# Kernel optimization log

Hardware: AMD Instinct MI355X
Metric: run time of the kernel (lower is better)

## Reference

```python
import jax, jax.numpy as jnp
import numpy as np

T, B, C, H, W, L, K = 8, 8, 64, 96, 96, 2, 3


def _conv(x, w):
    # x: [B,C,H,W], w: [O,I,K,K], SAME padding, stride 1
    return jax.lax.conv_general_dilated(
        x, w, window_strides=(1, 1), padding='SAME',
        dimension_numbers=('NCHW', 'OIHW', 'NCHW'))


def setup_inputs() -> dict:
    key = jax.random.key(0)
    ks = jax.random.split(key, 17)
    wscale = 0.04  # ~ 1/sqrt(64*9) fan-in
    out = {'x': jax.random.normal(ks[0], (T, B, C, H, W), jnp.float32)}
    wnames = ['wxi', 'whi', 'wci', 'wxf', 'whf', 'wcf', 'wxc', 'whc',
              'wxo', 'who', 'wco']
    for i, n in enumerate(wnames):
        out[n] = jax.random.normal(ks[1 + i], (L, C, C, K, K), jnp.float32) * wscale
    bnames = ['b_i', 'b_f', 'b_c', 'b_o']
    for i, n in enumerate(bnames):
        out[n] = jax.random.normal(ks[12 + i], (L, C), jnp.float32) * 0.01
    return out


def reference(x, wxi, whi, wci, wxf, whf, wcf, wxc, whc, wxo, who, wco,
              b_i, b_f, b_c, b_o):
    # x: [T,B,C,H,W]. Peephole Conv-LSTM; note original module's quirk:
    # output gate uses w_hc (with its bias) applied to the NEW cell state.
    hs = cs = None
    for l in range(L):
        Wxi, Whi, Wci = wxi[l], whi[l], wci[l]
        Wxf, Whf, Wcf = wxf[l], whf[l], wcf[l]
        Wxc, Whc = wxc[l], whc[l]
        Wxo, Who, Wco = wxo[l], who[l], wco[l]
        bi = b_i[l][None, :, None, None]
        bf = b_f[l][None, :, None, None]
        bc = b_c[l][None, :, None, None]
        bo = b_o[l][None, :, None, None]

        def step(carry, xt, Wxi=Wxi, Whi=Whi, Wci=Wci, Wxf=Wxf, Whf=Whf,
                 Wcf=Wcf, Wxc=Wxc, Whc=Whc, Wxo=Wxo, Who=Who,
                 bi=bi, bf=bf, bc=bc, bo=bo):
            h, c = carry
            i = jax.nn.sigmoid(_conv(xt, Wxi) + _conv(h, Whi) + bi + _conv(c, Wci))
            f = jax.nn.sigmoid(_conv(xt, Wxf) + _conv(h, Whf) + bf + _conv(c, Wcf))
            c_t = jnp.tanh(_conv(xt, Wxc) + _conv(h, Whc) + bc)
            c_new = c_t * i + c * f
            # faithful to source: w_hc (with its bias) on the new cell state
            o = jax.nn.sigmoid(_conv(xt, Wxo) + _conv(h, Who) + bo
                               + _conv(c_new, Whc) + bc)
            h_new = o * jnp.tanh(c_new)
            return (h_new, c_new), (h_new, c_new)

        h0 = jnp.zeros((x.shape[1], C, H, W), x.dtype)
        c0 = jnp.zeros((x.shape[1], C, H, W), x.dtype)
        _, (hs, cs) = jax.lax.scan(step, (h0, c0), x)
        x = hs  # next layer consumes this layer's hidden sequence
    return hs, cs  # each [T,B,C,H,W]
```

## Files before the change

kernel.cpp:

```cpp
#include <hip/hip_runtime.h>
#include <math.h>

#define TT 8
#define BB 8
#define CC 64
#define HH 96
#define WW 96
#define LL 2
#define HW   (HH * WW)
#define CHW  (CC * HW)
#define BCHW (BB * CHW)
#define TBCHW (TT * BCHW)
#define WSZ  (CC * CC * 9)

typedef _Float16 f16;
typedef __attribute__((ext_vector_type(8))) _Float16 f16x8;
typedef __attribute__((ext_vector_type(4))) _Float16 f16x4;
typedef __attribute__((ext_vector_type(4))) float f32x4;

__device__ __forceinline__ float sigmoidf_(float x) {
    return 1.0f / (1.0f + __expf(-x));
}


#define SLOT_B   9834496ull
#define PLANE_B  1229312ull
#define SLOT_F   (SLOT_B / 2)
#define GPLANE_F 4718592ull
#define WT_F     36864

struct WPtrs { const float* p[10]; };

__device__ __forceinline__ void gl_lds16(const void* g, void* lds_base) {
    __builtin_amdgcn_global_load_lds(
        (const __attribute__((address_space(1))) unsigned int*)g,
        (__attribute__((address_space(3))) unsigned int*)lds_base, 16, 0, 0);
}

__global__ __launch_bounds__(256) void wprep(WPtrs wsrcs, f16* Wf) {
    const int tap = blockIdx.x, ti = blockIdx.y, l = blockIdx.z;
    const float* src = wsrcs.p[ti] + l * WSZ;
    f16* dst = Wf + (size_t)(l * 10 + ti) * WT_F;
    for (int r = 0; r < 16; ++r) {
        int lin = r * 256 + threadIdx.x;
        int co = lin >> 6, ci = lin & 63;
        float v = src[(co * 64 + ci) * 9 + tap];
        int half = ci >> 5, e = ci & 31, s = e >> 3;
        int p = (s ^ co) & 3;
        dst[((half * 9 + tap) * 64 + co) * 32 + p * 8 + (e & 7)] = (f16)v;
    }
}

__global__ __launch_bounds__(256) void bzero(char* slots) {
    unsigned u = blockIdx.x * 256 + threadIdx.x;
    if (u >= 248320u) return;
    unsigned plane = u / 3104u;
    unsigned r = u % 3104u;
    unsigned i = r >> 3, c = r & 7;
    int y, x;
    if (i < 98)       { y = 0;           x = i; }
    else if (i < 196) { y = 97;          x = i - 98; }
    else if (i < 292) { y = i - 196 + 1; x = 0; }
    else              { y = i - 292 + 1; x = 97; }
    uint4 z = make_uint4(0, 0, 0, 0);
    *(uint4*)(slots + (size_t)plane * PLANE_B + (size_t)(y * 98 + x) * 128 + c * 16) = z;
}

__global__ __launch_bounds__(256) void xprep(const float* __restrict__ x, f16* slots) {
    const int t = blockIdx.y;
    const int b = blockIdx.x / 96, y = blockIdx.x % 96;
    f16* slot = slots + (size_t)t * SLOT_F;
    for (int r = 0; r < 3; ++r) {
        int u = r * 256 + threadIdx.x;
        int px = u >> 3, c = u & 7;
        int half = c >> 2, p = c & 3;
        int sc = (p ^ (px + 1)) & 3;
        int ci0 = half * 32 + sc * 8;
        const float* sp = x + ((((size_t)t * BB + b) * CC + ci0) * HH + y) * WW + px;
        union { f16 h[8]; uint4 q; } pk;
#pragma unroll
        for (int j = 0; j < 8; ++j) pk.h[j] = (f16)sp[(size_t)j * HW];
        f16* dp = slot + ((size_t)b * 9604 + (y + 1) * 98 + (px + 1)) * 64 + half * 32 + p * 8;
        *(uint4*)dp = pk.q;
    }
}

__device__ __forceinline__ void stage_phase(const char* __restrict__ xb_h, int y0,
                                            const char* __restrict__ wsec_h,
                                            int tid, f16* Xs, f16* Wl) {
    const int w = tid >> 6, lane = tid & 63;
    const char* xc = xb_h + (size_t)y0 * 12544;
    const int cb = w * 588;
#pragma unroll
    for (int i = 0; i < 9; ++i) {
        const int c = cb + i * 64 + lane;
        gl_lds16(xc + (size_t)(c >> 2) * 128 + (c & 3) * 16,
                 (char*)Xs + (size_t)(cb + i * 64) * 16);
    }
    if (lane < 12) {
        const int c = cb + 576 + lane;
        gl_lds16(xc + (size_t)(c >> 2) * 128 + (c & 3) * 16,
                 (char*)Xs + (size_t)(cb + 576) * 16);
    }
    const int cw = w * 576;
#pragma unroll
    for (int i = 0; i < 9; ++i) {
        gl_lds16(wsec_h + (size_t)(cw + i * 64 + lane) * 16,
                 (char*)Wl + (size_t)(cw + i * 64) * 16);
    }
}

__device__ __forceinline__ void mfma_phase(const f16* Xs, const f16* Wl,
                                           int w, int aBase, int d0, int d1, int d2,
                                           f32x4 acc[4][6]) {
#pragma unroll
    for (int tap = 0; tap < 9; ++tap) {
        const int dy = tap / 3, dx = tap % 3;
        const f16* Ar = &Wl[tap * 2048 + aBase];
        f16x8 a0 = *(const f16x8*)(Ar);
        f16x8 a1 = *(const f16x8*)(Ar + 512);
        f16x8 a2 = *(const f16x8*)(Ar + 1024);
        f16x8 a3 = *(const f16x8*)(Ar + 1536);
        const int doff = (dx == 0) ? d0 : (dx == 1) ? d1 : d2;
        const f16* Br = &Xs[(w + dy) * 3136 + doff];
#pragma unroll
        for (int nt = 0; nt < 6; ++nt) {
            f16x8 bf = *(const f16x8*)(Br + nt * 512);
            acc[0][nt] = __builtin_amdgcn_mfma_f32_16x16x32_f16(a0, bf, acc[0][nt], 0, 0, 0);
            acc[1][nt] = __builtin_amdgcn_mfma_f32_16x16x32_f16(a1, bf, acc[1][nt], 0, 0, 0);
            acc[2][nt] = __builtin_amdgcn_mfma_f32_16x16x32_f16(a2, bf, acc[2][nt], 0, 0, 0);
            acc[3][nt] = __builtin_amdgcn_mfma_f32_16x16x32_f16(a3, bf, acc[3][nt], 0, 0, 0);
        }
    }
}

struct GArgsN {
    const f16* in[3];
    const f16* w[4][3];
    f16* G;
};

__global__ __launch_bounds__(256) void gates_n(GArgsN A) {
    __shared__ __align__(16) f16 Xs[18816];
    __shared__ __align__(16) f16 Wl[18432];
    const int g = blockIdx.z, b = blockIdx.y, y0 = blockIdx.x * 4;
    const int tid = threadIdx.x, w = tid >> 6, lane = tid & 63;
    const int pxl = lane & 15, kg = lane >> 4;

    const int aBase = pxl * 32 + (((kg ^ pxl) & 3) << 3);
    const int d0 = (pxl + 0) * 32 + (((kg ^ (pxl + 0)) & 3) << 3);
    const int d1 = (pxl + 1) * 32 + (((kg ^ (pxl + 1)) & 3) << 3);
    const int d2 = (pxl + 2) * 32 + (((kg ^ (pxl + 2)) & 3) << 3);

    f32x4 acc[4][6];
#pragma unroll
    for (int mt = 0; mt < 4; ++mt)
#pragma unroll
        for (int nt = 0; nt < 6; ++nt) acc[mt][nt] = (f32x4){0.f, 0.f, 0.f, 0.f};

    for (int s = 0; s < 3; ++s) {
        const f16* xin = A.in[s];
        const f16* wsec = A.w[g][s];
        if (!xin || !wsec) continue;
        const char* xb = (const char*)(xin + (size_t)b * 614656);
        for (int h = 0; h < 2; ++h) {
            __syncthreads();
            stage_phase(xb + h * 64, y0, (const char*)(wsec + h * 18432), tid, Xs, Wl);
            __syncthreads();
            mfma_phase(Xs, Wl, w, aBase, d0, d1, d2, acc);
        }
    }

    f16* Gg = A.G + (size_t)g * GPLANE_F + ((size_t)b * 9216 + (y0 + w) * 96) * 64;
#pragma unroll
    for (int mt = 0; mt < 4; ++mt)
#pragma unroll
        for (int nt = 0; nt < 6; ++nt) {
            union { f16 h[4]; uint2 q; } pk;
#pragma unroll
            for (int r = 0; r < 4; ++r) pk.h[r] = (f16)acc[mt][nt][r];
            *(uint2*)(Gg + (size_t)(nt * 16 + pxl) * 64 + mt * 16 + kg * 4) = pk.q;
        }
}

__global__ __launch_bounds__(256) void pointwise_n(const f16* __restrict__ G,
                                                   const f16* __restrict__ cprev,
                                                   const float* __restrict__ bi,
                                                   const float* __restrict__ bf,
                                                   const float* __restrict__ bc,
                                                   f16* __restrict__ cnew,
                                                   float* __restrict__ cs_out) {
    const int b = blockIdx.y;
    const int u = blockIdx.x * 256 + threadIdx.x;
    const int pix = u >> 3, o = u & 7;
    const int ci0 = o * 8;
    const f16x8 gi = *(const f16x8*)(G + ((size_t)b * 9216 + pix) * 64 + ci0);
    const f16x8 gf = *(const f16x8*)(G + GPLANE_F + ((size_t)b * 9216 + pix) * 64 + ci0);
    const f16x8 gc = *(const f16x8*)(G + 2 * GPLANE_F + ((size_t)b * 9216 + pix) * 64 + ci0);
    const int py = pix / 96 + 1, pxp = pix % 96 + 1;
    const size_t pad_off = ((size_t)b * 9604 + py * 98 + pxp) * 64;
    const int half = o >> 2, p = ((o & 3) ^ pxp) & 3;
    const size_t sw_off = pad_off + half * 32 + p * 8;
    f16x8 cp = (f16x8)(_Float16)0.f;
    if (cprev) cp = *(const f16x8*)(cprev + sw_off);
    union { f16 h[8]; uint4 q; } outp;
    float cv[8];
#pragma unroll
    for (int j = 0; j < 8; ++j) {
        float vbi = bi[ci0 + j], vbf = bf[ci0 + j], vbc = bc[ci0 + j];
        float c = tanhf((float)gc[j] + vbc) * sigmoidf_((float)gi[j] + vbi)
                + (float)cp[j] * sigmoidf_((float)gf[j] + vbf);
        cv[j] = c;
        outp.h[j] = (f16)c;
    }
    *(uint4*)(cnew + sw_off) = outp.q;
    if (cs_out) {
        float* op = cs_out + (size_t)b * CHW + (size_t)ci0 * HW + pix;
#pragma unroll
        for (int j = 0; j < 8; ++j) op[(size_t)j * HW] = cv[j];
    }
}

__global__ __launch_bounds__(256) void out_n(const f16* __restrict__ cnew,
                                             const f16* __restrict__ whc,
                                             const f16* __restrict__ Go,
                                             const float* __restrict__ bo,
                                             const float* __restrict__ bc,
                                             f16* __restrict__ hslot,
                                             float* __restrict__ hs_out) {
    __shared__ __align__(16) f16 Xs[18816];
    __shared__ __align__(16) f16 Wl[18432];
    const int b = blockIdx.y, y0 = blockIdx.x * 4;
    const int tid = threadIdx.x, w = tid >> 6, lane = tid & 63;
    const int pxl = lane & 15, kg = lane >> 4;

    const int aBase = pxl * 32 + (((kg ^ pxl) & 3) << 3);
    const int d0 = (pxl + 0) * 32 + (((kg ^ (pxl + 0)) & 3) << 3);
    const int d1 = (pxl + 1) * 32 + (((kg ^ (pxl + 1)) & 3) << 3);
    const int d2 = (pxl + 2) * 32 + (((kg ^ (pxl + 2)) & 3) << 3);

    f32x4 acc[4][6];
#pragma unroll
    for (int mt = 0; mt < 4; ++mt)
#pragma unroll
        for (int nt = 0; nt < 6; ++nt) acc[mt][nt] = (f32x4){0.f, 0.f, 0.f, 0.f};

    const char* xb = (const char*)(cnew + (size_t)b * 614656);
    for (int h = 0; h < 2; ++h) {
        __syncthreads();
        stage_phase(xb + h * 64, y0, (const char*)(whc + h * 18432), tid, Xs, Wl);
        __syncthreads();
        mfma_phase(Xs, Wl, w, aBase, d0, d1, d2, acc);
    }

    const int y = y0 + w;
#pragma unroll
    for (int mt = 0; mt < 4; ++mt) {
        const int cob = mt * 16 + kg * 4;
        float vb[4];
#pragma unroll
        for (int r = 0; r < 4; ++r) vb[r] = bo[cob + r] + bc[cob + r];
        const int half = mt >> 1;
        const int sq = (mt * 2 + (kg >> 1)) & 3;
        const int lo4 = (kg & 1) * 4;
#pragma unroll
        for (int nt = 0; nt < 6; ++nt) {
            const int px = nt * 16 + pxl;
            const int pix = y * 96 + px;
            const size_t pad_off = ((size_t)b * 9604 + (y + 1) * 98 + (px + 1)) * 64;
            const int p = (sq ^ (px + 1)) & 3;
            const size_t qoff = pad_off + half * 32 + p * 8 + lo4;
            f16x4 cq = *(const f16x4*)(cnew + qoff);
            f16x4 gq = *(const f16x4*)(Go + ((size_t)b * 9216 + pix) * 64 + cob);
            union { f16 h[4]; uint2 q; } hq;
            float hv[4];
#pragma unroll
            for (int r = 0; r < 4; ++r) {
                float opre = acc[mt][nt][r] + (float)gq[r] + vb[r];
                hv[r] = sigmoidf_(opre) * tanhf((float)cq[r]);
                hq.h[r] = (f16)hv[r];
            }
            *(uint2*)(hslot + qoff) = hq.q;
            if (hs_out) {
                float* op = hs_out + (size_t)b * CHW + (size_t)cob * HW + pix;
#pragma unroll
                for (int r = 0; r < 4; ++r) op[(size_t)r * HW] = hv[r];
            }
        }
    }
}


#define XROW 3136
#define XSZ  (6 * XROW)
#define WROW 2048
#define WSZL (9 * WROW)

__device__ __forceinline__ void conv_section(
    const float* __restrict__ inb, const float* __restrict__ wp,
    int y0, int tid, f16* Xs, f16* Wl,
    int w, int aBase, int d0, int d1, int d2, f32x4 acc[4][6])
{
    for (int ci0 = 0; ci0 < 64; ci0 += 32) {
        __syncthreads();
        for (int i = tid; i < 9408; i += 256) {
            int x = i % 98; int r = i / 98; int yy = r % 6; int c2 = r / 6;
            int gy = y0 - 1 + yy, gx = x - 1;
            float v0 = 0.f, v1 = 0.f;
            if ((unsigned)gy < 96u && (unsigned)gx < 96u) {
                const float* p = inb + (size_t)(ci0 + 2 * c2) * HW + gy * WW + gx;
                v0 = p[0]; v1 = p[HW];
            }
            union { f16 h[2]; unsigned u; } pk;
            pk.h[0] = (f16)v0; pk.h[1] = (f16)v1;
            int e = 2 * c2;
            int idx = (yy * 98 + x) * 32 + ((((e >> 3) ^ x) & 3) << 3) + (e & 7);
            *(unsigned*)&Xs[idx] = pk.u;
        }
        for (int i = tid; i < 9216; i += 256) {
            int c2 = i & 15; int co = (i >> 4) & 63; int tap = i >> 10;
            const float* p = wp + ((size_t)co * CC + ci0 + 2 * c2) * 9 + tap;
            union { f16 h[2]; unsigned u; } pk;
            pk.h[0] = (f16)p[0]; pk.h[1] = (f16)p[9];
            int e = 2 * c2;
            int idx = tap * WROW + co * 32 + ((((e >> 3) ^ co) & 3) << 3) + (e & 7);
            *(unsigned*)&Wl[idx] = pk.u;
        }
        __syncthreads();
        mfma_phase(Xs, Wl, w, aBase, d0, d1, d2, acc);
    }
}

struct GArgs {
    const float* in[3];
    const float* w[4][3];
    f16* G;
};

__global__ __launch_bounds__(256) void gates_mfma(GArgs A) {
    __shared__ __align__(16) f16 Xs[XSZ];
    __shared__ __align__(16) f16 Wl[WSZL];
    const int g = blockIdx.z, b = blockIdx.y, y0 = blockIdx.x * 4;
    const int tid = threadIdx.x;
    const int w = tid >> 6, lane = tid & 63;
    const int pxl = lane & 15, kg = lane >> 4;
    const int aBase = pxl * 32 + (((kg ^ pxl) & 3) << 3);
    const int d0 = (pxl + 0) * 32 + (((kg ^ (pxl + 0)) & 3) << 3);
    const int d1 = (pxl + 1) * 32 + (((kg ^ (pxl + 1)) & 3) << 3);
    const int d2 = (pxl + 2) * 32 + (((kg ^ (pxl + 2)) & 3) << 3);
    f32x4 acc[4][6];
#pragma unroll
    for (int mt = 0; mt < 4; ++mt)
#pragma unroll
        for (int nt = 0; nt < 6; ++nt) acc[mt][nt] = (f32x4){0.f, 0.f, 0.f, 0.f};
    for (int s = 0; s < 3; ++s) {
        const float* inp = A.in[s];
        const float* wp = A.w[g][s];
        if (!inp || !wp) continue;
        conv_section(inp + (size_t)b * CHW, wp, y0, tid, Xs, Wl, w, aBase, d0, d1, d2, acc);
    }
    f16* Gp = A.G + (size_t)(g * BB + b) * CHW;
    const int y = y0 + w;
#pragma unroll
    for (int mt = 0; mt < 4; ++mt)
#pragma unroll
        for (int r = 0; r < 4; ++r) {
            const int co = mt * 16 + kg * 4 + r;
            f16* rp = Gp + (size_t)co * HW + y * WW + pxl;
#pragma unroll
            for (int nt = 0; nt < 6; ++nt) rp[nt * 16] = (f16)acc[mt][nt][r];
        }
}

__global__ __launch_bounds__(256) void pointwise_c(const f16* __restrict__ G,
                                                   const float* __restrict__ cprev,
                                                   const float* __restrict__ bi,
                                                   const float* __restrict__ bf,
                                                   const float* __restrict__ bc,
                                                   float* __restrict__ cnew) {
    int flat = (blockIdx.x * 256 + threadIdx.x) * 4;
    if (flat >= BCHW) return;
    int co = (flat / HW) & 63;
    f16x4 gi = *(const f16x4*)(G + flat);
    f16x4 gf = *(const f16x4*)(G + (size_t)BCHW + flat);
    f16x4 gc = *(const f16x4*)(G + 2 * (size_t)BCHW + flat);
    float4 cp = make_float4(0.f, 0.f, 0.f, 0.f);
    if (cprev) cp = *(const float4*)(cprev + flat);
    float vbi = bi[co], vbf = bf[co], vbc = bc[co];
    float4 r;
    r.x = tanhf((float)gc.x + vbc) * sigmoidf_((float)gi.x + vbi) + cp.x * sigmoidf_((float)gf.x + vbf);
    r.y = tanhf((float)gc.y + vbc) * sigmoidf_((float)gi.y + vbi) + cp.y * sigmoidf_((float)gf.y + vbf);
    r.z = tanhf((float)gc.z + vbc) * sigmoidf_((float)gi.z + vbi) + cp.z * sigmoidf_((float)gf.z + vbf);
    r.w = tanhf((float)gc.w + vbc) * sigmoidf_((float)gi.w + vbi) + cp.w * sigmoidf_((float)gf.w + vbf);
    *(float4*)(cnew + flat) = r;
}

__global__ __launch_bounds__(256) void out_mfma(const float* __restrict__ cnew,
                                                const float* __restrict__ wp,
                                                const f16* __restrict__ Go,
                                                const float* __restrict__ bo,
                                                const float* __restrict__ bc,
                                                float* __restrict__ hout) {
    __shared__ __align__(16) f16 Xs[XSZ];
    __shared__ __align__(16) f16 Wl[WSZL];
    const int b = blockIdx.y, y0 = blockIdx.x * 4;
    const int tid = threadIdx.x;
    const int w = tid >> 6, lane = tid & 63;
    const int pxl = lane & 15, kg = lane >> 4;
    const int aBase = pxl * 32 + (((kg ^ pxl) & 3) << 3);
    const int d0 = (pxl + 0) * 32 + (((kg ^ (pxl + 0)) & 3) << 3);
    const int d1 = (pxl + 1) * 32 + (((kg ^ (pxl + 1)) & 3) << 3);
    const int d2 = (pxl + 2) * 32 + (((kg ^ (pxl + 2)) & 3) << 3);
    f32x4 acc[4][6];
#pragma unroll
    for (int mt = 0; mt < 4; ++mt)
#pragma unroll
        for (int nt = 0; nt < 6; ++nt) acc[mt][nt] = (f32x4){0.f, 0.f, 0.f, 0.f};
    const float* cb = cnew + (size_t)b * CHW;
    conv_section(cb, wp, y0, tid, Xs, Wl, w, aBase, d0, d1, d2, acc);
    const f16* Gb = Go + (size_t)b * CHW;
    float* hb = hout + (size_t)b * CHW;
    const int y = y0 + w;
#pragma unroll
    for (int mt = 0; mt < 4; ++mt)
#pragma unroll
        for (int r = 0; r < 4; ++r) {
            const int co = mt * 16 + kg * 4 + r;
            const float vbv = bo[co] + bc[co];
            const size_t off0 = (size_t)co * HW + y * WW + pxl;
#pragma unroll
            for (int nt = 0; nt < 6; ++nt) {
                size_t off = off0 + nt * 16;
                float opre = acc[mt][nt][r] + (float)Gb[off] + vbv;
                hb[off] = sigmoidf_(opre) * tanhf(cb[off]);
            }
        }
}


extern "C" void kernel_launch(void* const* d_in, const int* in_sizes, int n_in,
                              void* d_out, int out_size, void* d_ws, size_t ws_size,
                              hipStream_t stream) {
    const float* x = (const float*)d_in[0];
    const float* w_[11];
    for (int i = 0; i < 11; ++i) w_[i] = (const float*)d_in[1 + i];
    const float* b_[4];
    for (int i = 0; i < 4; ++i) b_[i] = (const float*)d_in[12 + i];

    float* out = (float*)d_out;
    float* hs = out;
    float* cs = out + TBCHW;

    const size_t G_B = 4ull * GPLANE_F * 2ull;
    const size_t WF_B = 2ull * 10ull * WT_F * 2ull;
    const size_t NEED = 10ull * SLOT_B + G_B + WF_B;

    if (ws_size >= NEED) {
        char* ws = (char*)d_ws;
        f16* slots = (f16*)ws;
        f16* G = (f16*)(ws + 10ull * SLOT_B);
        f16* Wf = (f16*)(ws + 10ull * SLOT_B + G_B);

        WPtrs wps;
        for (int i = 0; i < 10; ++i) wps.p[i] = w_[i];

        wprep<<<dim3(9, 10, 2), 256, 0, stream>>>(wps, Wf);
        bzero<<<dim3(971), 256, 0, stream>>>((char*)slots);
        xprep<<<dim3(96 * BB, TT), 256, 0, stream>>>(x, slots);

        for (int l = 0; l < LL; ++l) {
            const f16* WT[10];
            for (int ti = 0; ti < 10; ++ti) WT[ti] = Wf + (size_t)(l * 10 + ti) * WT_F;
            const float* bi = b_[0] + l * CC;
            const float* bf = b_[1] + l * CC;
            const float* bc = b_[2] + l * CC;
            const float* bo = b_[3] + l * CC;

            for (int t = 0; t < TT; ++t) {
                f16* xt = slots + (size_t)t * SLOT_F;
                f16* hprev = (t == 0) ? nullptr : slots + (size_t)(t - 1) * SLOT_F;
                f16* cprev = (t == 0) ? nullptr
                                      : slots + (size_t)(8 + ((t - 1) & 1)) * SLOT_F;
                f16* cnew = slots + (size_t)(8 + (t & 1)) * SLOT_F;

                GArgsN a;
                a.in[0] = xt; a.in[1] = hprev; a.in[2] = cprev;
                a.w[0][0] = WT[0]; a.w[0][1] = WT[1]; a.w[0][2] = WT[2];
                a.w[1][0] = WT[3]; a.w[1][1] = WT[4]; a.w[1][2] = WT[5];
                a.w[2][0] = WT[6]; a.w[2][1] = WT[7]; a.w[2][2] = nullptr;
                a.w[3][0] = WT[8]; a.w[3][1] = WT[9]; a.w[3][2] = nullptr;
                a.G = G;
                gates_n<<<dim3(24, BB, 4), 256, 0, stream>>>(a);
                pointwise_n<<<dim3(288, BB), 256, 0, stream>>>(
                    G, cprev, bi, bf, bc, cnew,
                    (l == 1) ? (cs + (size_t)t * BCHW) : nullptr);
                out_n<<<dim3(24, BB), 256, 0, stream>>>(
                    cnew, WT[7], G + 3 * GPLANE_F, bo, bc,
                    xt,
                    (l == 1) ? (hs + (size_t)t * BCHW) : nullptr);
            }
        }
        return;
    }

    f16* G = (f16*)d_ws;
    float* c0 = (float*)d_ws + 2 * (size_t)BCHW;
    float* c1 = c0 + BCHW;

    for (int l = 0; l < LL; ++l) {
        const float* wxi = w_[0] + l * WSZ;
        const float* whi = w_[1] + l * WSZ;
        const float* wci = w_[2] + l * WSZ;
        const float* wxf = w_[3] + l * WSZ;
        const float* whf = w_[4] + l * WSZ;
        const float* wcf = w_[5] + l * WSZ;
        const float* wxc = w_[6] + l * WSZ;
        const float* whc = w_[7] + l * WSZ;
        const float* wxo = w_[8] + l * WSZ;
        const float* who = w_[9] + l * WSZ;
        const float* bi = b_[0] + l * CC;
        const float* bf = b_[1] + l * CC;
        const float* bc = b_[2] + l * CC;
        const float* bo = b_[3] + l * CC;

        for (int t = 0; t < TT; ++t) {
            const float* xt = (l == 0) ? (x + (size_t)t * BCHW) : (hs + (size_t)t * BCHW);
            const float* hprev = (t == 0) ? nullptr : (hs + (size_t)(t - 1) * BCHW);
            const float* cprev = (t == 0) ? nullptr
                : (l == 0 ? (((t - 1) & 1) ? c1 : c0) : (cs + (size_t)(t - 1) * BCHW));
            float* cnew = (l == 0) ? ((t & 1) ? c1 : c0) : (cs + (size_t)t * BCHW);

            GArgs a;
            a.in[0] = xt; a.in[1] = hprev; a.in[2] = cprev;
            a.w[0][0] = wxi; a.w[0][1] = whi; a.w[0][2] = wci;
            a.w[1][0] = wxf; a.w[1][1] = whf; a.w[1][2] = wcf;
            a.w[2][0] = wxc; a.w[2][1] = whc; a.w[2][2] = nullptr;
            a.w[3][0] = wxo; a.w[3][1] = who; a.w[3][2] = nullptr;
            a.G = G;
            gates_mfma<<<dim3(24, BB, 4), 256, 0, stream>>>(a);
            pointwise_c<<<dim3(BCHW / 1024), 256, 0, stream>>>(G, cprev, bi, bf, bc, cnew);
            out_mfma<<<dim3(24, BB), 256, 0, stream>>>(cnew, whc, G + (size_t)3 * BCHW,
                                                       bo, bc, hs + (size_t)t * BCHW);
        }
    }
}
```

Measured before the change: 1.815 ms.

## Prefetch conv weights through registers one phase ahead; use fast tanh

The per-phase LDS staging of weights is split out. Weights for the next phase are now loaded into registers while the current phase's MFMAs run, then written to LDS at the start of the next phase, overlapping weight fetch latency with compute. The t=0 null-pointer skipping is replaced by a zeroed slot that is re-zeroed at the start of each layer, so the kernels take fixed templated phase counts with no per-section branches. This does more convolution work at the first timestep. tanhf is replaced by an exp-based approximation in the pointwise and output kernels, which can lose accuracy or overflow to inf for large inputs, though the formula still saturates to ±1.

```diff
diff --git a/kernel.cpp b/kernel.cpp
--- a/kernel.cpp
+++ b/kernel.cpp
@@ -20,6 +20,10 @@
 
 __device__ __forceinline__ float sigmoidf_(float x) {
     return 1.0f / (1.0f + __expf(-x));
+}
+__device__ __forceinline__ float tanhf_(float x) {
+    float e = __expf(2.f * x);
+    return 1.f - 2.f / (e + 1.f);
 }
 
 
@@ -66,6 +70,11 @@
     *(uint4*)(slots + (size_t)plane * PLANE_B + (size_t)(y * 98 + x) * 128 + c * 16) = z;
 }
 
+__global__ __launch_bounds__(256) void zslot(char* slot) {
+    size_t off = ((size_t)blockIdx.x * 256 + threadIdx.x) * 16;
+    *(uint4*)(slot + off) = make_uint4(0, 0, 0, 0);
+}
+
 __global__ __launch_bounds__(256) void xprep(const float* __restrict__ x, f16* slots) {
     const int t = blockIdx.y;
     const int b = blockIdx.x / 96, y = blockIdx.x % 96;
@@ -85,10 +94,8 @@
     }
 }
 
-__device__ __forceinline__ void stage_phase(const char* __restrict__ xb_h, int y0,
-                                            const char* __restrict__ wsec_h,
-                                            int tid, f16* Xs, f16* Wl) {
-    const int w = tid >> 6, lane = tid & 63;
+__device__ __forceinline__ void stage_x(const char* __restrict__ xb_h, int y0,
+                                        int w, int lane, f16* Xs) {
     const char* xc = xb_h + (size_t)y0 * 12544;
     const int cb = w * 588;
 #pragma unroll
@@ -102,12 +109,20 @@
         gl_lds16(xc + (size_t)(c >> 2) * 128 + (c & 3) * 16,
                  (char*)Xs + (size_t)(cb + 576) * 16);
     }
-    const int cw = w * 576;
-#pragma unroll
-    for (int i = 0; i < 9; ++i) {
-        gl_lds16(wsec_h + (size_t)(cw + i * 64 + lane) * 16,
-                 (char*)Wl + (size_t)(cw + i * 64) * 16);
-    }
+}
+
+struct W9 { uint4 v[9]; };
+__device__ __forceinline__ W9 wload(const char* __restrict__ wsec_h, int cw, int lane) {
+    W9 r;
+#pragma unroll
+    for (int i = 0; i < 9; ++i)
+        r.v[i] = *(const uint4*)(wsec_h + (size_t)(cw + i * 64 + lane) * 16);
+    return r;
+}
+__device__ __forceinline__ void wstore(f16* Wl, const W9& r, int cw, int lane) {
+#pragma unroll
+    for (int i = 0; i < 9; ++i)
+        *(uint4*)((char*)Wl + (size_t)(cw + i * 64 + lane) * 16) = r.v[i];
 }
 
 __device__ __forceinline__ void mfma_phase(const f16* Xs, const f16* Wl,
@@ -134,6 +149,30 @@
     }
 }
 
+template<int NP>
+__device__ __forceinline__ void conv_pipe(const char* xb0, const char* xb1, const char* xb2,
+                                          const char* wp0, const char* wp1, const char* wp2,
+                                          int y0, int w, int lane, int cw,
+                                          f16* Xs, f16* Wl,
+                                          int aBase, int d0, int d1, int d2,
+                                          f32x4 acc[4][6]) {
+    W9 wreg = wload(wp0, cw, lane);
+#pragma unroll
+    for (int p = 0; p < NP; ++p) {
+        const char* xb_s = ((p >> 1) == 0) ? xb0 : ((p >> 1) == 1) ? xb1 : xb2;
+        __syncthreads();
+        wstore(Wl, wreg, cw, lane);
+        stage_x(xb_s + (p & 1) * 64, y0, w, lane, Xs);
+        __syncthreads();
+        if (p + 1 < NP) {
+            const int s1 = (p + 1) >> 1;
+            const char* wp_s = (s1 == 0) ? wp0 : (s1 == 1) ? wp1 : wp2;
+            wreg = wload(wp_s + ((p + 1) & 1) * 36864, cw, lane);
+        }
+        mfma_phase(Xs, Wl, w, aBase, d0, d1, d2, acc);
+    }
+}
+
 struct GArgsN {
     const f16* in[3];
     const f16* w[4][3];
@@ -146,6 +185,7 @@
     const int g = blockIdx.z, b = blockIdx.y, y0 = blockIdx.x * 4;
     const int tid = threadIdx.x, w = tid >> 6, lane = tid & 63;
     const int pxl = lane & 15, kg = lane >> 4;
+    const int cw = w * 576;
 
     const int aBase = pxl * 32 + (((kg ^ pxl) & 3) << 3);
     const int d0 = (pxl + 0) * 32 + (((kg ^ (pxl + 0)) & 3) << 3);
@@ -158,18 +198,19 @@
 #pragma unroll
         for (int nt = 0; nt < 6; ++nt) acc[mt][nt] = (f32x4){0.f, 0.f, 0.f, 0.f};
 
-    for (int s = 0; s < 3; ++s) {
-        const f16* xin = A.in[s];
-        const f16* wsec = A.w[g][s];
-        if (!xin || !wsec) continue;
-        const char* xb = (const char*)(xin + (size_t)b * 614656);
-        for (int h = 0; h < 2; ++h) {
-            __syncthreads();
-            stage_phase(xb + h * 64, y0, (const char*)(wsec + h * 18432), tid, Xs, Wl);
-            __syncthreads();
-            mfma_phase(Xs, Wl, w, aBase, d0, d1, d2, acc);
-        }
-    }
+    const char* xb0 = (const char*)(A.in[0] + (size_t)b * 614656);
+    const char* xb1 = (const char*)(A.in[1] + (size_t)b * 614656);
+    const char* xb2 = (const char*)(A.in[2] + (size_t)b * 614656);
+    const char* wp0 = (const char*)A.w[g][0];
+    const char* wp1 = (const char*)A.w[g][1];
+    const char* wp2 = (const char*)A.w[g][2];
+
+    if (g < 2)
+        conv_pipe<6>(xb0, xb1, xb2, wp0, wp1, wp2, y0, w, lane, cw,
+                     Xs, Wl, aBase, d0, d1, d2, acc);
+    else
+        conv_pipe<4>(xb0, xb1, xb2, wp0, wp1, wp2, y0, w, lane, cw,
+                     Xs, Wl, aBase, d0, d1, d2, acc);
 
     f16* Gg = A.G + (size_t)g * GPLANE_F + ((size_t)b * 9216 + (y0 + w) * 96) * 64;
 #pragma unroll
@@ -201,14 +242,13 @@
     const size_t pad_off = ((size_t)b * 9604 + py * 98 + pxp) * 64;
     const int half = o >> 2, p = ((o & 3) ^ pxp) & 3;
     const size_t sw_off = pad_off + half * 32 + p * 8;
-    f16x8 cp = (f16x8)(_Float16)0.f;
-    if (cprev) cp = *(const f16x8*)(cprev + sw_off);
+    const f16x8 cp = *(const f16x8*)(cprev + sw_off);
     union { f16 h[8]; uint4 q; } outp;
     float cv[8];
 #pragma unroll
     for (int j = 0; j < 8; ++j) {
         float vbi = bi[ci0 + j], vbf = bf[ci0 + j], vbc = bc[ci0 + j];
-        float c = tanhf((float)gc[j] + vbc) * sigmoidf_((float)gi[j] + vbi)
+        float c = tanhf_((float)gc[j] + vbc) * sigmoidf_((float)gi[j] + vbi)
                 + (float)cp[j] * sigmoidf_((float)gf[j] + vbf);
         cv[j] = c;
         outp.h[j] = (f16)c;
@@ -233,6 +273,7 @@
     const int b = blockIdx.y, y0 = blockIdx.x * 4;
     const int tid = threadIdx.x, w = tid >> 6, lane = tid & 63;
     const int pxl = lane & 15, kg = lane >> 4;
+    const int cw = w * 576;
 
     const int aBase = pxl * 32 + (((kg ^ pxl) & 3) << 3);
     const int d0 = (pxl + 0) * 32 + (((kg ^ (pxl + 0)) & 3) << 3);
@@ -246,12 +287,8 @@
         for (int nt = 0; nt < 6; ++nt) acc[mt][nt] = (f32x4){0.f, 0.f, 0.f, 0.f};
 
     const char* xb = (const char*)(cnew + (size_t)b * 614656);
-    for (int h = 0; h < 2; ++h) {
-        __syncthreads();
-        stage_phase(xb + h * 64, y0, (const char*)(whc + h * 18432), tid, Xs, Wl);
-        __syncthreads();
-        mfma_phase(Xs, Wl, w, aBase, d0, d1, d2, acc);
-    }
+    conv_pipe<2>(xb, xb, xb, (const char*)whc, (const char*)whc, (const char*)whc,
+                 y0, w, lane, cw, Xs, Wl, aBase, d0, d1, d2, acc);
 
     const int y = y0 + w;
 #pragma unroll
@@ -277,7 +314,7 @@
 #pragma unroll
             for (int r = 0; r < 4; ++r) {
                 float opre = acc[mt][nt][r] + (float)gq[r] + vb[r];
-                hv[r] = sigmoidf_(opre) * tanhf((float)cq[r]);
+                hv[r] = sigmoidf_(opre) * tanhf_((float)cq[r]);
                 hq.h[r] = (f16)hv[r];
             }
             *(uint2*)(hslot + qoff) = hq.q;
@@ -388,10 +425,10 @@
     if (cprev) cp = *(const float4*)(cprev + flat);
     float vbi = bi[co], vbf = bf[co], vbc = bc[co];
     float4 r;
-    r.x = tanhf((float)gc.x + vbc) * sigmoidf_((float)gi.x + vbi) + cp.x * sigmoidf_((float)gf.x + vbf);
-    r.y = tanhf((float)gc.y + vbc) * sigmoidf_((float)gi.y + vbi) + cp.y * sigmoidf_((float)gf.y + vbf);
-    r.z = tanhf((float)gc.z + vbc) * sigmoidf_((float)gi.z + vbi) + cp.z * sigmoidf_((float)gf.z + vbf);
-    r.w = tanhf((float)gc.w + vbc) * sigmoidf_((float)gi.w + vbi) + cp.w * sigmoidf_((float)gf.w + vbf);
+    r.x = tanhf_((float)gc.x + vbc) * sigmoidf_((float)gi.x + vbi) + cp.x * sigmoidf_((float)gf.x + vbf);
+    r.y = tanhf_((float)gc.y + vbc) * sigmoidf_((float)gi.y + vbi) + cp.y * sigmoidf_((float)gf.y + vbf);
+    r.z = tanhf_((float)gc.z + vbc) * sigmoidf_((float)gi.z + vbi) + cp.z * sigmoidf_((float)gf.z + vbf);
+    r.w = tanhf_((float)gc.w + vbc) * sigmoidf_((float)gi.w + vbi) + cp.w * sigmoidf_((float)gf.w + vbf);
     *(float4*)(cnew + flat) = r;
 }
 
@@ -432,7 +469,7 @@
             for (int nt = 0; nt < 6; ++nt) {
                 size_t off = off0 + nt * 16;
                 float opre = acc[mt][nt][r] + (float)Gb[off] + vbv;
-                hb[off] = sigmoidf_(opre) * tanhf(cb[off]);
+                hb[off] = sigmoidf_(opre) * tanhf_(cb[off]);
             }
         }
 }
@@ -460,6 +497,7 @@
         f16* slots = (f16*)ws;
         f16* G = (f16*)(ws + 10ull * SLOT_B);
         f16* Wf = (f16*)(ws + 10ull * SLOT_B + G_B);
+        f16* zc = slots + 9ull * SLOT_F;
 
         WPtrs wps;
         for (int i = 0; i < 10; ++i) wps.p[i] = w_[i];
@@ -469,6 +507,8 @@
         xprep<<<dim3(96 * BB, TT), 256, 0, stream>>>(x, slots);
 
         for (int l = 0; l < LL; ++l) {
+            zslot<<<dim3(2401), 256, 0, stream>>>((char*)zc);
+
             const f16* WT[10];
             for (int ti = 0; ti < 10; ++ti) WT[ti] = Wf + (size_t)(l * 10 + ti) * WT_F;
             const float* bi = b_[0] + l * CC;
@@ -478,17 +518,16 @@
 
             for (int t = 0; t < TT; ++t) {
                 f16* xt = slots + (size_t)t * SLOT_F;
-                f16* hprev = (t == 0) ? nullptr : slots + (size_t)(t - 1) * SLOT_F;
-                f16* cprev = (t == 0) ? nullptr
-                                      : slots + (size_t)(8 + ((t - 1) & 1)) * SLOT_F;
+                f16* hprev = (t == 0) ? zc : slots + (size_t)(t - 1) * SLOT_F;
+                f16* cprev = (t == 0) ? zc : slots + (size_t)(8 + ((t - 1) & 1)) * SLOT_F;
                 f16* cnew = slots + (size_t)(8 + (t & 1)) * SLOT_F;
 
                 GArgsN a;
                 a.in[0] = xt; a.in[1] = hprev; a.in[2] = cprev;
                 a.w[0][0] = WT[0]; a.w[0][1] = WT[1]; a.w[0][2] = WT[2];
                 a.w[1][0] = WT[3]; a.w[1][1] = WT[4]; a.w[1][2] = WT[5];
-                a.w[2][0] = WT[6]; a.w[2][1] = WT[7]; a.w[2][2] = nullptr;
-                a.w[3][0] = WT[8]; a.w[3][1] = WT[9]; a.w[3][2] = nullptr;
+                a.w[2][0] = WT[6]; a.w[2][1] = WT[7]; a.w[2][2] = WT[6];
+                a.w[3][0] = WT[8]; a.w[3][1] = WT[9]; a.w[3][2] = WT[8];
                 a.G = G;
                 gates_n<<<dim3(24, BB, 4), 256, 0, stream>>>(a);
                 pointwise_n<<<dim3(288, BB), 256, 0, stream>>>(
```

Result: slower. 3.031 ms (+67.0%).

## Read conv weights directly from global memory, shrink LDS, raise occupancy

Applied to the files above, without the earlier changes.

The gates and output conv kernels no longer stage weight tiles into shared memory. MFMA A-operands are loaded straight from global memory, which roughly halves LDS use per block and lets launch_bounds request 3 blocks per CU. The gate index moves into blockIdx.x so the four gates for the same rows run as adjacent blocks and can share cached input and weight data. tanhf is also replaced by an exp-based approximation. The trade-off is extra global/L2 traffic on the MFMA path, and the approximate tanh risks small accuracy differences.

```diff
diff --git a/kernel.cpp b/kernel.cpp
--- a/kernel.cpp
+++ b/kernel.cpp
@@ -20,6 +20,10 @@
 
 __device__ __forceinline__ float sigmoidf_(float x) {
     return 1.0f / (1.0f + __expf(-x));
+}
+__device__ __forceinline__ float tanhf_(float x) {
+    float e = __expf(2.f * x);
+    return 1.f - 2.f / (e + 1.f);
 }
 
 
@@ -85,10 +89,8 @@
     }
 }
 
-__device__ __forceinline__ void stage_phase(const char* __restrict__ xb_h, int y0,
-                                            const char* __restrict__ wsec_h,
-                                            int tid, f16* Xs, f16* Wl) {
-    const int w = tid >> 6, lane = tid & 63;
+__device__ __forceinline__ void stage_x(const char* __restrict__ xb_h, int y0,
+                                        int w, int lane, f16* Xs) {
     const char* xc = xb_h + (size_t)y0 * 12544;
     const int cb = w * 588;
 #pragma unroll
@@ -102,21 +104,15 @@
         gl_lds16(xc + (size_t)(c >> 2) * 128 + (c & 3) * 16,
                  (char*)Xs + (size_t)(cb + 576) * 16);
     }
-    const int cw = w * 576;
-#pragma unroll
-    for (int i = 0; i < 9; ++i) {
-        gl_lds16(wsec_h + (size_t)(cw + i * 64 + lane) * 16,
-                 (char*)Wl + (size_t)(cw + i * 64) * 16);
-    }
-}
-
-__device__ __forceinline__ void mfma_phase(const f16* Xs, const f16* Wl,
-                                           int w, int aBase, int d0, int d1, int d2,
-                                           f32x4 acc[4][6]) {
+}
+
+__device__ __forceinline__ void mfma_phase_g(const f16* Xs, const f16* __restrict__ wph,
+                                             int w, int aBase, int d0, int d1, int d2,
+                                             f32x4 acc[4][6]) {
 #pragma unroll
     for (int tap = 0; tap < 9; ++tap) {
         const int dy = tap / 3, dx = tap % 3;
-        const f16* Ar = &Wl[tap * 2048 + aBase];
+        const f16* Ar = wph + tap * 2048 + aBase;
         f16x8 a0 = *(const f16x8*)(Ar);
         f16x8 a1 = *(const f16x8*)(Ar + 512);
         f16x8 a2 = *(const f16x8*)(Ar + 1024);
@@ -140,10 +136,9 @@
     f16* G;
 };
 
-__global__ __launch_bounds__(256) void gates_n(GArgsN A) {
+__global__ __launch_bounds__(256, 3) void gates_n(GArgsN A) {
     __shared__ __align__(16) f16 Xs[18816];
-    __shared__ __align__(16) f16 Wl[18432];
-    const int g = blockIdx.z, b = blockIdx.y, y0 = blockIdx.x * 4;
+    const int g = blockIdx.x & 3, b = blockIdx.y, y0 = (blockIdx.x >> 2) * 4;
     const int tid = threadIdx.x, w = tid >> 6, lane = tid & 63;
     const int pxl = lane & 15, kg = lane >> 4;
 
@@ -165,9 +160,9 @@
         const char* xb = (const char*)(xin + (size_t)b * 614656);
         for (int h = 0; h < 2; ++h) {
             __syncthreads();
-            stage_phase(xb + h * 64, y0, (const char*)(wsec + h * 18432), tid, Xs, Wl);
+            stage_x(xb + h * 64, y0, w, lane, Xs);
             __syncthreads();
-            mfma_phase(Xs, Wl, w, aBase, d0, d1, d2, acc);
+            mfma_phase_g(Xs, wsec + h * 18432, w, aBase, d0, d1, d2, acc);
         }
     }
 
@@ -208,7 +203,7 @@
 #pragma unroll
     for (int j = 0; j < 8; ++j) {
         float vbi = bi[ci0 + j], vbf = bf[ci0 + j], vbc = bc[ci0 + j];
-        float c = tanhf((float)gc[j] + vbc) * sigmoidf_((float)gi[j] + vbi)
+        float c = tanhf_((float)gc[j] + vbc) * sigmoidf_((float)gi[j] + vbi)
                 + (float)cp[j] * sigmoidf_((float)gf[j] + vbf);
         cv[j] = c;
         outp.h[j] = (f16)c;
@@ -221,15 +216,14 @@
     }
 }
 
-__global__ __launch_bounds__(256) void out_n(const f16* __restrict__ cnew,
-                                             const f16* __restrict__ whc,
-                                             const f16* __restrict__ Go,
-                                             const float* __restrict__ bo,
-                                             const float* __restrict__ bc,
-                                             f16* __restrict__ hslot,
-                                             float* __restrict__ hs_out) {
+__global__ __launch_bounds__(256, 3) void out_n(const f16* __restrict__ cnew,
+                                                const f16* __restrict__ whc,
+                                                const f16* __restrict__ Go,
+                                                const float* __restrict__ bo,
+                                                const float* __restrict__ bc,
+                                                f16* __restrict__ hslot,
+                                                float* __restrict__ hs_out) {
     __shared__ __align__(16) f16 Xs[18816];
-    __shared__ __align__(16) f16 Wl[18432];
     const int b = blockIdx.y, y0 = blockIdx.x * 4;
     const int tid = threadIdx.x, w = tid >> 6, lane = tid & 63;
     const int pxl = lane & 15, kg = lane >> 4;
@@ -248,9 +242,9 @@
     const char* xb = (const char*)(cnew + (size_t)b * 614656);
     for (int h = 0; h < 2; ++h) {
         __syncthreads();
-        stage_phase(xb + h * 64, y0, (const char*)(whc + h * 18432), tid, Xs, Wl);
+        stage_x(xb + h * 64, y0, w, lane, Xs);
         __syncthreads();
-        mfma_phase(Xs, Wl, w, aBase, d0, d1, d2, acc);
+        mfma_phase_g(Xs, whc + h * 18432, w, aBase, d0, d1, d2, acc);
     }
 
     const int y = y0 + w;
@@ -277,7 +271,7 @@
 #pragma unroll
             for (int r = 0; r < 4; ++r) {
                 float opre = acc[mt][nt][r] + (float)gq[r] + vb[r];
-                hv[r] = sigmoidf_(opre) * tanhf((float)cq[r]);
+                hv[r] = sigmoidf_(opre) * tanhf_((float)cq[r]);
                 hq.h[r] = (f16)hv[r];
             }
             *(uint2*)(hslot + qoff) = hq.q;
@@ -295,6 +289,30 @@
 #define XSZ  (6 * XROW)
 #define WROW 2048
 #define WSZL (9 * WROW)
+
+__device__ __forceinline__ void mfma_phase(const f16* Xs, const f16* Wl,
+                                           int w, int aBase, int d0, int d1, int d2,
+                                           f32x4 acc[4][6]) {
+#pragma unroll
+    for (int tap = 0; tap < 9; ++tap) {
+        const int dy = tap / 3, dx = tap % 3;
+        const f16* Ar = &Wl[tap * 2048 + aBase];
+        f16x8 a0 = *(const f16x8*)(Ar);
+        f16x8 a1 = *(const f16x8*)(Ar + 512);
+        f16x8 a2 = *(const f16x8*)(Ar + 1024);
+        f16x8 a3 = *(const f16x8*)(Ar + 1536);
+        const int doff = (dx == 0) ? d0 : (dx == 1) ? d1 : d2;
+        const f16* Br = &Xs[(w + dy) * 3136 + doff];
+#pragma unroll
+        for (int nt = 0; nt < 6; ++nt) {
+            f16x8 bf = *(const f16x8*)(Br + nt * 512);
+            acc[0][nt] = __builtin_amdgcn_mfma_f32_16x16x32_f16(a0, bf, acc[0][nt], 0, 0, 0);
+            acc[1][nt] = __builtin_amdgcn_mfma_f32_16x16x32_f16(a1, bf, acc[1][nt], 0, 0, 0);
+            acc[2][nt] = __builtin_amdgcn_mfma_f32_16x16x32_f16(a2, bf, acc[2][nt], 0, 0, 0);
+            acc[3][nt] = __builtin_amdgcn_mfma_f32_16x16x32_f16(a3, bf, acc[3][nt], 0, 0, 0);
+        }
+    }
+}
 
 __device__ __forceinline__ void conv_section(
     const float* __restrict__ inb, const float* __restrict__ wp,
@@ -388,10 +406,10 @@
     if (cprev) cp = *(const float4*)(cprev + flat);
     float vbi = bi[co], vbf = bf[co], vbc = bc[co];
     float4 r;
-    r.x = tanhf((float)gc.x + vbc) * sigmoidf_((float)gi.x + vbi) + cp.x * sigmoidf_((float)gf.x + vbf);
-    r.y = tanhf((float)gc.y + vbc) * sigmoidf_((float)gi.y + vbi) + cp.y * sigmoidf_((float)gf.y + vbf);
-    r.z = tanhf((float)gc.z + vbc) * sigmoidf_((float)gi.z + vbi) + cp.z * sigmoidf_((float)gf.z + vbf);
-    r.w = tanhf((float)gc.w + vbc) * sigmoidf_((float)gi.w + vbi) + cp.w * sigmoidf_((float)gf.w + vbf);
+    r.x = tanhf_((float)gc.x + vbc) * sigmoidf_((float)gi.x + vbi) + cp.x * sigmoidf_((float)gf.x + vbf);
+    r.y = tanhf_((float)gc.y + vbc) * sigmoidf_((float)gi.y + vbi) + cp.y * sigmoidf_((float)gf.y + vbf);
+    r.z = tanhf_((float)gc.z + vbc) * sigmoidf_((float)gi.z + vbi) + cp.z * sigmoidf_((float)gf.z + vbf);
+    r.w = tanhf_((float)gc.w + vbc) * sigmoidf_((float)gi.w + vbi) + cp.w * sigmoidf_((float)gf.w + vbf);
     *(float4*)(cnew + flat) = r;
 }
 
@@ -432,7 +450,7 @@
             for (int nt = 0; nt < 6; ++nt) {
                 size_t off = off0 + nt * 16;
                 float opre = acc[mt][nt][r] + (float)Gb[off] + vbv;
-                hb[off] = sigmoidf_(opre) * tanhf(cb[off]);
+                hb[off] = sigmoidf_(opre) * tanhf_(cb[off]);
             }
         }
 }
@@ -490,7 +508,7 @@
                 a.w[2][0] = WT[6]; a.w[2][1] = WT[7]; a.w[2][2] = nullptr;
                 a.w[3][0] = WT[8]; a.w[3][1] = WT[9]; a.w[3][2] = nullptr;
                 a.G = G;
-                gates_n<<<dim3(24, BB, 4), 256, 0, stream>>>(a);
+                gates_n<<<dim3(96, BB), 256, 0, stream>>>(a);
                 pointwise_n<<<dim3(288, BB), 256, 0, stream>>>(
                     G, cprev, bi, bf, bc, cnew,
                     (l == 1) ? (cs + (size_t)t * BCHW) : nullptr);
```

After: 2.200 ms. 1.21x slower.

## Double-buffer LDS staging in gate and output conv kernels, fast tanh

Applied to the files above, without the earlier changes.

The gate and output convolution kernels now keep two LDS buffers, so the async global-to-LDS load for the next channel half or section is issued while MFMAs run on the current one, and one barrier per phase is removed. The grid is flattened to 1D with batch as the fastest index, and the section count is passed explicitly so the t==0 step skips the h and c sections. tanhf is replaced by an exp-based approximation. Doubling LDS to about 146KB per block with launch_bounds(256,1) limits occupancy to one block per CU, which reduces latency hiding between blocks.

```diff
diff --git a/kernel.cpp b/kernel.cpp
--- a/kernel.cpp
+++ b/kernel.cpp
@@ -21,6 +21,10 @@
 __device__ __forceinline__ float sigmoidf_(float x) {
     return 1.0f / (1.0f + __expf(-x));
 }
+__device__ __forceinline__ float tanhf_(float x) {
+    float e = __expf(2.f * x);
+    return 1.f - 2.f / (e + 1.f);
+}
 
 
 #define SLOT_B   9834496ull
@@ -28,6 +32,8 @@
 #define SLOT_F   (SLOT_B / 2)
 #define GPLANE_F 4718592ull
 #define WT_F     36864
+#define XHALF_F  18816
+#define WHALF_F  18432
 
 struct WPtrs { const float* p[10]; };
 
@@ -87,8 +93,7 @@
 
 __device__ __forceinline__ void stage_phase(const char* __restrict__ xb_h, int y0,
                                             const char* __restrict__ wsec_h,
-                                            int tid, f16* Xs, f16* Wl) {
-    const int w = tid >> 6, lane = tid & 63;
+                                            int w, int lane, f16* Xs, f16* Wl) {
     const char* xc = xb_h + (size_t)y0 * 12544;
     const int cb = w * 588;
 #pragma unroll
@@ -138,12 +143,14 @@
     const f16* in[3];
     const f16* w[4][3];
     f16* G;
+    int nsecA, nsecB;
 };
 
-__global__ __launch_bounds__(256) void gates_n(GArgsN A) {
-    __shared__ __align__(16) f16 Xs[18816];
-    __shared__ __align__(16) f16 Wl[18432];
-    const int g = blockIdx.z, b = blockIdx.y, y0 = blockIdx.x * 4;
+__global__ __launch_bounds__(256, 1) void gates_n(GArgsN A) {
+    __shared__ __align__(16) f16 Xs[2 * XHALF_F];
+    __shared__ __align__(16) f16 Wl[2 * WHALF_F];
+    const int bid = blockIdx.x;
+    const int b = bid & 7, rr = bid >> 3, g = rr & 3, y0 = (rr >> 2) * 4;
     const int tid = threadIdx.x, w = tid >> 6, lane = tid & 63;
     const int pxl = lane & 15, kg = lane >> 4;
 
@@ -158,17 +165,28 @@
 #pragma unroll
         for (int nt = 0; nt < 6; ++nt) acc[mt][nt] = (f32x4){0.f, 0.f, 0.f, 0.f};
 
-    for (int s = 0; s < 3; ++s) {
-        const f16* xin = A.in[s];
-        const f16* wsec = A.w[g][s];
-        if (!xin || !wsec) continue;
-        const char* xb = (const char*)(xin + (size_t)b * 614656);
-        for (int h = 0; h < 2; ++h) {
-            __syncthreads();
-            stage_phase(xb + h * 64, y0, (const char*)(wsec + h * 18432), tid, Xs, Wl);
-            __syncthreads();
-            mfma_phase(Xs, Wl, w, aBase, d0, d1, d2, acc);
-        }
+    const char* xb0 = (const char*)(A.in[0] + (size_t)b * 614656);
+    const char* xb1 = (const char*)(A.in[1] + (size_t)b * 614656);
+    const char* xb2 = (const char*)(A.in[2] + (size_t)b * 614656);
+    const char* wp0 = (const char*)A.w[g][0];
+    const char* wp1 = (const char*)A.w[g][1];
+    const char* wp2 = (const char*)A.w[g][2];
+    const int NP = 2 * ((g < 2) ? A.nsecA : A.nsecB);
+
+    stage_phase(xb0, y0, wp0, w, lane, Xs, Wl);
+    __syncthreads();
+    for (int p = 0; p < NP; ++p) {
+        const int cur = p & 1;
+        if (p + 1 < NP) {
+            const int s1 = (p + 1) >> 1, h1 = (p + 1) & 1;
+            const char* xb_s = (s1 == 0) ? xb0 : (s1 == 1) ? xb1 : xb2;
+            const char* wp_s = (s1 == 0) ? wp0 : (s1 == 1) ? wp1 : wp2;
+            stage_phase(xb_s + h1 * 64, y0, wp_s + h1 * 36864, w, lane,
+                        Xs + (cur ^ 1) * XHALF_F, Wl + (cur ^ 1) * WHALF_F);
+        }
+        mfma_phase(Xs + cur * XHALF_F, Wl + cur * WHALF_F,
+                   w, aBase, d0, d1, d2, acc);
+        __syncthreads();
     }
 
     f16* Gg = A.G + (size_t)g * GPLANE_F + ((size_t)b * 9216 + (y0 + w) * 96) * 64;
@@ -208,7 +226,7 @@
 #pragma unroll
     for (int j = 0; j < 8; ++j) {
         float vbi = bi[ci0 + j], vbf = bf[ci0 + j], vbc = bc[ci0 + j];
-        float c = tanhf((float)gc[j] + vbc) * sigmoidf_((float)gi[j] + vbi)
+        float c = tanhf_((float)gc[j] + vbc) * sigmoidf_((float)gi[j] + vbi)
                 + (float)cp[j] * sigmoidf_((float)gf[j] + vbf);
         cv[j] = c;
         outp.h[j] = (f16)c;
@@ -221,16 +239,17 @@
     }
 }
 
-__global__ __launch_bounds__(256) void out_n(const f16* __restrict__ cnew,
-                                             const f16* __restrict__ whc,
-                                             const f16* __restrict__ Go,
-                                             const float* __restrict__ bo,
-                                             const float* __restrict__ bc,
-                                             f16* __restrict__ hslot,
-                                             float* __restrict__ hs_out) {
-    __shared__ __align__(16) f16 Xs[18816];
-    __shared__ __align__(16) f16 Wl[18432];
-    const int b = blockIdx.y, y0 = blockIdx.x * 4;
+__global__ __launch_bounds__(256, 1) void out_n(const f16* __restrict__ cnew,
+                                                const f16* __restrict__ whc,
+                                                const f16* __restrict__ Go,
+                                                const float* __restrict__ bo,
+                                                const float* __restrict__ bc,
+                                                f16* __restrict__ hslot,
+                                                float* __restrict__ hs_out) {
+    __shared__ __align__(16) f16 Xs[2 * XHALF_F];
+    __shared__ __align__(16) f16 Wl[2 * WHALF_F];
+    const int bid = blockIdx.x;
+    const int b = bid & 7, y0 = (bid >> 3) * 4;
     const int tid = threadIdx.x, w = tid >> 6, lane = tid & 63;
     const int pxl = lane & 15, kg = lane >> 4;
 
@@ -246,11 +265,16 @@
         for (int nt = 0; nt < 6; ++nt) acc[mt][nt] = (f32x4){0.f, 0.f, 0.f, 0.f};
 
     const char* xb = (const char*)(cnew + (size_t)b * 614656);
-    for (int h = 0; h < 2; ++h) {
+    stage_phase(xb, y0, (const char*)whc, w, lane, Xs, Wl);
+    __syncthreads();
+    for (int p = 0; p < 2; ++p) {
+        const int cur = p & 1;
+        if (p == 0)
+            stage_phase(xb + 64, y0, (const char*)whc + 36864, w, lane,
+                        Xs + XHALF_F, Wl + WHALF_F);
+        mfma_phase(Xs + cur * XHALF_F, Wl + cur * WHALF_F,
+                   w, aBase, d0, d1, d2, acc);
         __syncthreads();
-        stage_phase(xb + h * 64, y0, (const char*)(whc + h * 18432), tid, Xs, Wl);
-        __syncthreads();
-        mfma_phase(Xs, Wl, w, aBase, d0, d1, d2, acc);
     }
 
     const int y = y0 + w;
@@ -277,7 +301,7 @@
 #pragma unroll
             for (int r = 0; r < 4; ++r) {
                 float opre = acc[mt][nt][r] + (float)gq[r] + vb[r];
-                hv[r] = sigmoidf_(opre) * tanhf((float)cq[r]);
+                hv[r] = sigmoidf_(opre) * tanhf_((float)cq[r]);
                 hq.h[r] = (f16)hv[r];
             }
             *(uint2*)(hslot + qoff) = hq.q;
@@ -388,10 +412,10 @@
     if (cprev) cp = *(const float4*)(cprev + flat);
     float vbi = bi[co], vbf = bf[co], vbc = bc[co];
     float4 r;
-    r.x = tanhf((float)gc.x + vbc) * sigmoidf_((float)gi.x + vbi) + cp.x * sigmoidf_((float)gf.x + vbf);
-    r.y = tanhf((float)gc.y + vbc) * sigmoidf_((float)gi.y + vbi) + cp.y * sigmoidf_((float)gf.y + vbf);
-    r.z = tanhf((float)gc.z + vbc) * sigmoidf_((float)gi.z + vbi) + cp.z * sigmoidf_((float)gf.z + vbf);
-    r.w = tanhf((float)gc.w + vbc) * sigmoidf_((float)gi.w + vbi) + cp.w * sigmoidf_((float)gf.w + vbf);
+    r.x = tanhf_((float)gc.x + vbc) * sigmoidf_((float)gi.x + vbi) + cp.x * sigmoidf_((float)gf.x + vbf);
+    r.y = tanhf_((float)gc.y + vbc) * sigmoidf_((float)gi.y + vbi) + cp.y * sigmoidf_((float)gf.y + vbf);
+    r.z = tanhf_((float)gc.z + vbc) * sigmoidf_((float)gi.z + vbi) + cp.z * sigmoidf_((float)gf.z + vbf);
+    r.w = tanhf_((float)gc.w + vbc) * sigmoidf_((float)gi.w + vbi) + cp.w * sigmoidf_((float)gf.w + vbf);
     *(float4*)(cnew + flat) = r;
 }
 
@@ -432,7 +456,7 @@
             for (int nt = 0; nt < 6; ++nt) {
                 size_t off = off0 + nt * 16;
                 float opre = acc[mt][nt][r] + (float)Gb[off] + vbv;
-                hb[off] = sigmoidf_(opre) * tanhf(cb[off]);
+                hb[off] = sigmoidf_(opre) * tanhf_(cb[off]);
             }
         }
 }
@@ -484,17 +508,27 @@
                 f16* cnew = slots + (size_t)(8 + (t & 1)) * SLOT_F;
 
                 GArgsN a;
-                a.in[0] = xt; a.in[1] = hprev; a.in[2] = cprev;
-                a.w[0][0] = WT[0]; a.w[0][1] = WT[1]; a.w[0][2] = WT[2];
-                a.w[1][0] = WT[3]; a.w[1][1] = WT[4]; a.w[1][2] = WT[5];
-                a.w[2][0] = WT[6]; a.w[2][1] = WT[7]; a.w[2][2] = nullptr;
-                a.w[3][0] = WT[8]; a.w[3][1] = WT[9]; a.w[3][2] = nullptr;
+                if (t == 0) {
+                    a.in[0] = xt; a.in[1] = xt; a.in[2] = xt;
+                    a.w[0][0] = WT[0]; a.w[0][1] = WT[0]; a.w[0][2] = WT[0];
+                    a.w[1][0] = WT[3]; a.w[1][1] = WT[3]; a.w[1][2] = WT[3];
+                    a.w[2][0] = WT[6]; a.w[2][1] = WT[6]; a.w[2][2] = WT[6];
+                    a.w[3][0] = WT[8]; a.w[3][1] = WT[8]; a.w[3][2] = WT[8];
+                    a.nsecA = 1; a.nsecB = 1;
+                } else {
+                    a.in[0] = xt; a.in[1] = hprev; a.in[2] = cprev;
+                    a.w[0][0] = WT[0]; a.w[0][1] = WT[1]; a.w[0][2] = WT[2];
+                    a.w[1][0] = WT[3]; a.w[1][1] = WT[4]; a.w[1][2] = WT[5];
+                    a.w[2][0] = WT[6]; a.w[2][1] = WT[7]; a.w[2][2] = WT[7];
+                    a.w[3][0] = WT[8]; a.w[3][1] = WT[9]; a.w[3][2] = WT[9];
+                    a.nsecA = 3; a.nsecB = 2;
+                }
                 a.G = G;
-                gates_n<<<dim3(24, BB, 4), 256, 0, stream>>>(a);
+                gates_n<<<dim3(768), 256, 0, stream>>>(a);
                 pointwise_n<<<dim3(288, BB), 256, 0, stream>>>(
                     G, cprev, bi, bf, bc, cnew,
                     (l == 1) ? (cs + (size_t)t * BCHW) : nullptr);
-                out_n<<<dim3(24, BB), 256, 0, stream>>>(
+                out_n<<<dim3(192), 256, 0, stream>>>(
                     cnew, WT[7], G + 3 * GPLANE_F, bo, bc,
                     xt,
                     (l == 1) ? (hs + (size_t)t * BCHW) : nullptr);
```

After: 1.716 ms (median of 2 runs). 5.5% less time.
